# Kernel tuning notes

Hardware: AMD Instinct MI355X
Metric: run time of the kernel (lower is better)

## Reference

```python
import jax, jax.numpy as jnp
import numpy as np

N = 200000      # number of source simplices (columns of B)
M_SEG = 100000  # number of target simplices (rows of B)
NNZ = 400000    # ~2 nonzeros per column for a boundary operator
C_IN = 256
C_OUT = 256


def setup_inputs() -> dict:
    key = jax.random.key(0)
    k1, k2, k3, k4, k5 = jax.random.split(key, 5)
    x_src = jax.random.normal(k1, (N, C_IN), dtype=jnp.float32)
    W = jax.random.normal(k2, (C_IN, C_OUT), dtype=jnp.float32) / np.sqrt(C_IN)
    b_vals = jax.random.normal(k3, (NNZ,), dtype=jnp.float32)
    b_rows = jax.random.randint(k4, (NNZ,), 0, M_SEG, dtype=jnp.int32)
    b_cols = jax.random.randint(k5, (NNZ,), 0, N, dtype=jnp.int32)
    return {"x_src": x_src, "W": W, "b_vals": b_vals,
            "b_rows": b_rows, "b_cols": b_cols, "M": M_SEG}


def reference(x_src, W, b_vals, b_rows, b_cols, M):
    # Dense projection: nn.Linear(in, out, bias=False) -> x @ W
    x_proj = x_src @ W                                  # [N, C_out]
    # Sparse boundary matmul: out[r] += v * x_proj[c] for each (r, c, v) in B
    msgs = b_vals[:, None] * x_proj[b_cols]             # [nnz, C_out] gather
    out = jax.ops.segment_sum(msgs, b_rows, num_segments=M)  # [M, C_out] scatter-add
    return out
```

## Files before the change

### kernel.cpp

```cpp
#include <hip/hip_runtime.h>


typedef short bf16x8 __attribute__((ext_vector_type(8)));
typedef float f32x4  __attribute__((ext_vector_type(4)));

#define PGRID 256

static __device__ __forceinline__ unsigned short f2bf(float f) {
    union { float f; unsigned u; } a; a.f = f;
    unsigned r = a.u + 0x7FFFu + ((a.u >> 16) & 1u);
    return (unsigned short)(r >> 16);
}

static __device__ __forceinline__ float bf2f(unsigned short h) {
    union { unsigned u; float f; } a; a.u = (unsigned)h << 16;
    return a.f;
}

static __device__ __forceinline__ unsigned pack2(float f0, float f1) {
    return (unsigned)f2bf(f0) | ((unsigned)f2bf(f1) << 16);
}

static __device__ __forceinline__ bf16x8 cvt8(float4 lo, float4 hi) {
    union { bf16x8 v; unsigned u[4]; } r;
    r.u[0] = pack2(lo.x, lo.y);
    r.u[1] = pack2(lo.z, lo.w);
    r.u[2] = pack2(hi.x, hi.y);
    r.u[3] = pack2(hi.z, hi.w);
    return r.v;
}

static __device__ __forceinline__ void gload_lds16(const void* g, void* l) {
    __builtin_amdgcn_global_load_lds(
        (const __attribute__((address_space(1))) unsigned int*)g,
        (__attribute__((address_space(3))) unsigned int*)l,
        16, 0, 0);
}

__global__ __launch_bounds__(256) void wtrans_kernel(
    const float* __restrict__ W, unsigned short* __restrict__ Wt)
{
    int k = blockIdx.x;
    int n = threadIdx.x;
    Wt[(size_t)n * 256 + k] = f2bf(W[(size_t)k * 256 + n]);
}

__global__ __launch_bounds__(256) void hist_kernel(
    const int* __restrict__ b_rows, int* __restrict__ cnt, int nnz)
{
    int i = blockIdx.x * 256 + threadIdx.x;
    if (i < nnz) atomicAdd(&cnt[b_rows[i]], 1);
}

__global__ __launch_bounds__(1024) void scan_part_kernel(
    const int* __restrict__ cnt, int* __restrict__ partials, int M)
{
    int tid = threadIdx.x;
    int base = blockIdx.x * 4096;
    int s = 0;
    #pragma unroll
    for (int k = 0; k < 4; ++k) {
        int i = base + k * 1024 + tid;
        if (i < M) s += cnt[i];
    }
    #pragma unroll
    for (int d = 1; d < 64; d <<= 1) s += __shfl_xor(s, d);
    __shared__ int wsum[16];
    int lane = tid & 63, wid = tid >> 6;
    if (lane == 0) wsum[wid] = s;
    __syncthreads();
    if (tid == 0) {
        int t = 0;
        #pragma unroll
        for (int w = 0; w < 16; ++w) t += wsum[w];
        partials[blockIdx.x] = t;
    }
}

__global__ __launch_bounds__(64) void scan_mid_kernel(
    int* __restrict__ partials, int* __restrict__ off, int np, int M)
{
    int lane = threadIdx.x;
    int v = (lane < np) ? partials[lane] : 0;
    int x = v;
    #pragma unroll
    for (int d = 1; d < 64; d <<= 1) { int y = __shfl_up(x, d); if (lane >= d) x += y; }
    if (lane < np) partials[lane] = x - v;
    if (lane == 63) off[M] = x;
}

__global__ __launch_bounds__(1024) void scan_apply_kernel(
    const int* __restrict__ cnt, const int* __restrict__ partials,
    int* __restrict__ off, int* __restrict__ cursor, int M)
{
    int tid = threadIdx.x;
    int base = blockIdx.x * 4096 + tid * 4;
    int4 v = make_int4(0, 0, 0, 0);
    if (base + 3 < M) v = *reinterpret_cast<const int4*>(cnt + base);
    else {
        if (base + 0 < M) v.x = cnt[base + 0];
        if (base + 1 < M) v.y = cnt[base + 1];
        if (base + 2 < M) v.z = cnt[base + 2];
    }
    int s1 = v.x + v.y, s2 = s1 + v.z, tsum = s2 + v.w;
    int x = tsum;
    int lane = tid & 63, wid = tid >> 6;
    #pragma unroll
    for (int d = 1; d < 64; d <<= 1) { int y = __shfl_up(x, d); if (lane >= d) x += y; }
    __shared__ int wsum[16];
    if (lane == 63) wsum[wid] = x;
    __syncthreads();
    if (wid == 0 && lane < 16) {
        int w = wsum[lane];
        int xx = w;
        #pragma unroll
        for (int d = 1; d < 16; d <<= 1) { int y = __shfl_up(xx, d); if (lane >= d) xx += y; }
        wsum[lane] = xx - w;
    }
    __syncthreads();
    int excl = (x - tsum) + wsum[wid] + partials[blockIdx.x];
    int o0 = excl, o1 = excl + v.x, o2 = excl + s1, o3 = excl + s2;
    if (base + 0 < M) { off[base + 0] = o0; cursor[base + 0] = o0; }
    if (base + 1 < M) { off[base + 1] = o1; cursor[base + 1] = o1; }
    if (base + 2 < M) { off[base + 2] = o2; cursor[base + 2] = o2; }
    if (base + 3 < M) { off[base + 3] = o3; cursor[base + 3] = o3; }
}

__global__ __launch_bounds__(256) void fill_kernel(
    const float* __restrict__ b_vals, const int* __restrict__ b_rows,
    const int* __restrict__ b_cols, int* __restrict__ cursor,
    int* __restrict__ csr_col, float* __restrict__ csr_val, int nnz)
{
    int i = blockIdx.x * 256 + threadIdx.x;
    if (i < nnz) {
        int r = b_rows[i];
        int pos = atomicAdd(&cursor[r], 1);
        csr_col[pos] = b_cols[i];
        csr_val[pos] = b_vals[i];
    }
}

__global__ __launch_bounds__(512, 2) void proj3_kernel(
    const float* __restrict__ X, const unsigned short* __restrict__ Wt,
    unsigned short* __restrict__ xp, int ntiles)
{
    __shared__ __align__(16) unsigned char abuf[2][2][16 * 1024];

    int tid = threadIdx.x;
    int lane = tid & 63, w = tid >> 6;
    int grp = w >> 2;
    int ww  = w & 3;
    int arow = lane & 15;
    int kg = lane >> 4;

    bf16x8 b[4][8];
    {
        const char* wt = reinterpret_cast<const char*>(Wt);
        size_t nb = (size_t)(ww * 64 + arow) * 512 + kg * 16;
        #pragma unroll
        for (int nt = 0; nt < 4; ++nt)
            #pragma unroll
            for (int s = 0; s < 8; ++s)
                b[nt][s] = *reinterpret_cast<const bf16x8*>(
                    wt + nb + (size_t)nt * 16 * 512 + s * 64);
    }

    const char* Xb = reinterpret_cast<const char*>(X);
    int gid = blockIdx.x * 2 + grp;
    const int stride = PGRID * 2;
    int rounds = (ntiles + stride - 1) / stride;

    int swz = (lane * 16);

    {
        int tile = gid;
        if (tile < ntiles) {
            #pragma unroll
            for (int ii = 0; ii < 4; ++ii) {
                int i = ww * 4 + ii;
                const void* src = Xb + (size_t)(tile * 16 + i) * 1024
                                     + (swz ^ ((i & 7) << 4));
                gload_lds16(src, &abuf[0][grp][i * 1024]);
            }
        }
    }
    __syncthreads();

    for (int r = 0; r < rounds; ++r) {
        int tile = gid + r * stride;
        int p = r & 1;

        {
            int ntile = gid + (r + 1) * stride;
            if (ntile < ntiles) {
                #pragma unroll
                for (int ii = 0; ii < 4; ++ii) {
                    int i = ww * 4 + ii;
                    const void* src = Xb + (size_t)(ntile * 16 + i) * 1024
                                         + (swz ^ ((i & 7) << 4));
                    gload_lds16(src, &abuf[p ^ 1][grp][i * 1024]);
                }
            }
        }

        if (tile < ntiles) {
            const unsigned char* ab = abuf[p][grp];
            int rx = arow * 1024;
            int xo = (arow & 7) << 4;
            f32x4 acc[4] = {};
            #pragma unroll
            for (int s = 0; s < 8; ++s) {
                int base = kg * 32 + s * 128;
                float4 lo = *reinterpret_cast<const float4*>(ab + rx + ((base +  0) ^ xo));
                float4 hi = *reinterpret_cast<const float4*>(ab + rx + ((base + 16) ^ xo));
                bf16x8 a = cvt8(lo, hi);
                #pragma unroll
                for (int nt = 0; nt < 4; ++nt)
                    acc[nt] = __builtin_amdgcn_mfma_f32_16x16x32_bf16(a, b[nt][s], acc[nt], 0, 0, 0);
            }
            int R = tile * 16;
            #pragma unroll
            for (int rr = 0; rr < 4; ++rr) {
                int row = R + kg * 4 + rr;
                ushort4 h;
                h.x = f2bf(acc[0][rr]);
                h.y = f2bf(acc[1][rr]);
                h.z = f2bf(acc[2][rr]);
                h.w = f2bf(acc[3][rr]);
                *reinterpret_cast<ushort4*>(xp + (size_t)row * 256 + ww * 64 + arow * 4) = h;
            }
        }
        __syncthreads();
    }
}

__global__ __launch_bounds__(256) void gather_kernel(
    const unsigned short* __restrict__ xp, const float* __restrict__ csr_val,
    const int* __restrict__ csr_col, const int* __restrict__ off,
    float* __restrict__ out, int M)
{
    __shared__ float obuf[4][256];

    int wid = threadIdx.x >> 6;
    int row = blockIdx.x * 4 + wid;
    if (row >= M) return;
    int lane = threadIdx.x & 63;

    int s = off[row], e = off[row + 1];
    float a0 = 0.f, a1 = 0.f, a2 = 0.f, a3 = 0.f;

    for (int j = s; j < e; j += 8) {
        int nb = e - j;
        int c[8]; float v[8]; ushort4 xs[8];
        #pragma unroll
        for (int t = 0; t < 8; ++t)
            if (t < nb) { c[t] = csr_col[j + t]; v[t] = csr_val[j + t]; }
        #pragma unroll
        for (int t = 0; t < 8; ++t)
            if (t < nb)
                xs[t] = *reinterpret_cast<const ushort4*>(
                    xp + (size_t)c[t] * 256 + lane * 4);
        #pragma unroll
        for (int t = 0; t < 8; ++t)
            if (t < nb) {
                a0 += v[t] * bf2f(xs[t].x);
                a1 += v[t] * bf2f(xs[t].y);
                a2 += v[t] * bf2f(xs[t].z);
                a3 += v[t] * bf2f(xs[t].w);
            }
    }

    int col0 = (lane >> 4) * 64 + (lane & 15);
    obuf[wid][col0 +  0] = a0;
    obuf[wid][col0 + 16] = a1;
    obuf[wid][col0 + 32] = a2;
    obuf[wid][col0 + 48] = a3;
    float4 o = *reinterpret_cast<const float4*>(&obuf[wid][lane * 4]);
    *reinterpret_cast<float4*>(out + (size_t)row * 256 + lane * 4) = o;
}

extern "C" void kernel_launch(void* const* d_in, const int* in_sizes, int n_in,
                              void* d_out, int out_size, void* d_ws, size_t ws_size,
                              hipStream_t stream) {
    const float* x_src  = (const float*)d_in[0];
    const float* W      = (const float*)d_in[1];
    const float* b_vals = (const float*)d_in[2];
    const int*   b_rows = (const int*)d_in[3];
    const int*   b_cols = (const int*)d_in[4];

    const int C = 256;
    const int M = out_size / C;
    const int nnz = in_sizes[2];
    const int N = in_sizes[0] / C;

    char* ws = (char*)d_ws;
    unsigned short* Wt = (unsigned short*)ws;           ws += 256 * 256 * 2;
    int*   cnt     = (int*)ws;                          ws += (size_t)M * 4;
    int*   off     = (int*)ws;                          ws += (size_t)(M + 1) * 4;
    int*   cursor  = (int*)ws;                          ws += (size_t)M * 4;
    int*   partials= (int*)ws;                          ws += 64 * 4;
    int*   csr_col = (int*)ws;                          ws += (size_t)nnz * 4;
    float* csr_val = (float*)ws;                        ws += (size_t)nnz * 4;
    ws = (char*)(((size_t)ws + 63) & ~(size_t)63);
    unsigned short* xp = (unsigned short*)ws;

    float* out = (float*)d_out;

    hipMemsetAsync(cnt, 0, (size_t)M * 4, stream);

    wtrans_kernel<<<256, 256, 0, stream>>>(W, Wt);

    int nblk_nnz = (nnz + 255) / 256;
    hist_kernel<<<nblk_nnz, 256, 0, stream>>>(b_rows, cnt, nnz);

    int nb = (M + 4095) / 4096;
    scan_part_kernel<<<nb, 1024, 0, stream>>>(cnt, partials, M);
    scan_mid_kernel<<<1, 64, 0, stream>>>(partials, off, nb, M);
    scan_apply_kernel<<<nb, 1024, 0, stream>>>(cnt, partials, off, cursor, M);

    fill_kernel<<<nblk_nnz, 256, 0, stream>>>(b_vals, b_rows, b_cols, cursor,
                                              csr_col, csr_val, nnz);

    int ntiles = N / 16;
    proj3_kernel<<<PGRID, 512, 0, stream>>>(x_src, Wt, xp, ntiles);

    gather_kernel<<<(M + 3) / 4, 256, 0, stream>>>(xp, csr_val, csr_col, off, out, M);
}
```

Before: 198.6 us.

## Split projection tile across eight waves with fewer B registers, raise grid

The projection kernel now processes one 16-row tile per block, with each of the eight waves computing 32 output columns instead of four waves computing 64. This halves the per-wave W fragment registers and allows four blocks per CU and a 1024-block grid, aiming for higher occupancy and better latency hiding of the X streaming. The xp column layout changes to interleave pairs, and the gather kernel's output permutation is updated to match. The trade-off is that each X tile in LDS is now converted to bf16 by all eight waves, which duplicates the conversion work.

```diff
diff --git a/kernel.cpp b/kernel.cpp
--- a/kernel.cpp
+++ b/kernel.cpp
@@ -4,7 +4,7 @@
 typedef short bf16x8 __attribute__((ext_vector_type(8)));
 typedef float f32x4  __attribute__((ext_vector_type(4)));
 
-#define PGRID 256
+#define PGRID 1024
 
 static __device__ __forceinline__ unsigned short f2bf(float f) {
     union { float f; unsigned u; } a; a.f = f;
@@ -140,94 +140,82 @@
     }
 }
 
-__global__ __launch_bounds__(512, 2) void proj3_kernel(
+__global__ __launch_bounds__(512, 4) void proj5_kernel(
     const float* __restrict__ X, const unsigned short* __restrict__ Wt,
     unsigned short* __restrict__ xp, int ntiles)
 {
-    __shared__ __align__(16) unsigned char abuf[2][2][16 * 1024];
+    __shared__ __align__(16) unsigned char abuf[2][16 * 1024];
 
     int tid = threadIdx.x;
     int lane = tid & 63, w = tid >> 6;
-    int grp = w >> 2;
-    int ww  = w & 3;
     int arow = lane & 15;
     int kg = lane >> 4;
 
-    bf16x8 b[4][8];
+    bf16x8 b[2][8];
     {
         const char* wt = reinterpret_cast<const char*>(Wt);
-        size_t nb = (size_t)(ww * 64 + arow) * 512 + kg * 16;
-        #pragma unroll
-        for (int nt = 0; nt < 4; ++nt)
+        #pragma unroll
+        for (int nt = 0; nt < 2; ++nt) {
+            size_t nb = (size_t)(w * 32 + nt * 16 + arow) * 512 + kg * 16;
             #pragma unroll
             for (int s = 0; s < 8; ++s)
-                b[nt][s] = *reinterpret_cast<const bf16x8*>(
-                    wt + nb + (size_t)nt * 16 * 512 + s * 64);
+                b[nt][s] = *reinterpret_cast<const bf16x8*>(wt + nb + s * 64);
+        }
     }
 
     const char* Xb = reinterpret_cast<const char*>(X);
-    int gid = blockIdx.x * 2 + grp;
-    const int stride = PGRID * 2;
-    int rounds = (ntiles + stride - 1) / stride;
-
-    int swz = (lane * 16);
+    int swz = lane * 16;
+    int rounds = (ntiles + PGRID - 1) / PGRID;
 
     {
-        int tile = gid;
-        if (tile < ntiles) {
-            #pragma unroll
-            for (int ii = 0; ii < 4; ++ii) {
-                int i = ww * 4 + ii;
-                const void* src = Xb + (size_t)(tile * 16 + i) * 1024
-                                     + (swz ^ ((i & 7) << 4));
-                gload_lds16(src, &abuf[0][grp][i * 1024]);
-            }
+        int tile = blockIdx.x;
+        #pragma unroll
+        for (int ii = 0; ii < 2; ++ii) {
+            int i = w * 2 + ii;
+            const void* src = Xb + (size_t)(tile * 16 + i) * 1024
+                                 + (swz ^ ((i & 7) << 4));
+            gload_lds16(src, &abuf[0][i * 1024]);
         }
     }
     __syncthreads();
 
     for (int r = 0; r < rounds; ++r) {
-        int tile = gid + r * stride;
+        int tile = blockIdx.x + r * PGRID;
         int p = r & 1;
 
         {
-            int ntile = gid + (r + 1) * stride;
+            int ntile = tile + PGRID;
             if (ntile < ntiles) {
                 #pragma unroll
-                for (int ii = 0; ii < 4; ++ii) {
-                    int i = ww * 4 + ii;
+                for (int ii = 0; ii < 2; ++ii) {
+                    int i = w * 2 + ii;
                     const void* src = Xb + (size_t)(ntile * 16 + i) * 1024
                                          + (swz ^ ((i & 7) << 4));
-                    gload_lds16(src, &abuf[p ^ 1][grp][i * 1024]);
+                    gload_lds16(src, &abuf[p ^ 1][i * 1024]);
                 }
             }
         }
 
         if (tile < ntiles) {
-            const unsigned char* ab = abuf[p][grp];
+            const unsigned char* ab = abuf[p];
             int rx = arow * 1024;
             int xo = (arow & 7) << 4;
-            f32x4 acc[4] = {};
+            f32x4 acc0 = {}, acc1 = {};
             #pragma unroll
             for (int s = 0; s < 8; ++s) {
                 int base = kg * 32 + s * 128;
                 float4 lo = *reinterpret_cast<const float4*>(ab + rx + ((base +  0) ^ xo));
                 float4 hi = *reinterpret_cast<const float4*>(ab + rx + ((base + 16) ^ xo));
                 bf16x8 a = cvt8(lo, hi);
-                #pragma unroll
-                for (int nt = 0; nt < 4; ++nt)
-                    acc[nt] = __builtin_amdgcn_mfma_f32_16x16x32_bf16(a, b[nt][s], acc[nt], 0, 0, 0);
+                acc0 = __builtin_amdgcn_mfma_f32_16x16x32_bf16(a, b[0][s], acc0, 0, 0, 0);
+                acc1 = __builtin_amdgcn_mfma_f32_16x16x32_bf16(a, b[1][s], acc1, 0, 0, 0);
             }
             int R = tile * 16;
             #pragma unroll
             for (int rr = 0; rr < 4; ++rr) {
                 int row = R + kg * 4 + rr;
-                ushort4 h;
-                h.x = f2bf(acc[0][rr]);
-                h.y = f2bf(acc[1][rr]);
-                h.z = f2bf(acc[2][rr]);
-                h.w = f2bf(acc[3][rr]);
-                *reinterpret_cast<ushort4*>(xp + (size_t)row * 256 + ww * 64 + arow * 4) = h;
+                *reinterpret_cast<unsigned*>(xp + (size_t)row * 256 + w * 32 + arow * 2)
+                    = pack2(acc0[rr], acc1[rr]);
             }
         }
         __syncthreads();
@@ -270,11 +258,11 @@
             }
     }
 
-    int col0 = (lane >> 4) * 64 + (lane & 15);
-    obuf[wid][col0 +  0] = a0;
-    obuf[wid][col0 + 16] = a1;
-    obuf[wid][col0 + 32] = a2;
-    obuf[wid][col0 + 48] = a3;
+    int cbase = (lane >> 3) * 32 + (lane & 7) * 2;
+    obuf[wid][cbase +  0] = a0;
+    obuf[wid][cbase + 16] = a1;
+    obuf[wid][cbase +  1] = a2;
+    obuf[wid][cbase + 17] = a3;
     float4 o = *reinterpret_cast<const float4*>(&obuf[wid][lane * 4]);
     *reinterpret_cast<float4*>(out + (size_t)row * 256 + lane * 4) = o;
 }
@@ -322,7 +310,7 @@
                                               csr_col, csr_val, nnz);
 
     int ntiles = N / 16;
-    proj3_kernel<<<PGRID, 512, 0, stream>>>(x_src, Wt, xp, ntiles);
+    proj5_kernel<<<PGRID, 512, 0, stream>>>(x_src, Wt, xp, ntiles);
 
     gather_kernel<<<(M + 3) / 4, 256, 0, stream>>>(xp, csr_val, csr_col, off, out, M);
 }
```

After: 207.4 us. 1.04x slower.
